# Performance work log

Measured on AMD Instinct MI355X. Metric: run time of the kernel, lower is better.

Reference implementation:

```python
import jax, jax.numpy as jnp
import numpy as np


def setup_inputs() -> dict:
    key = jax.random.key(0)
    k1, k2 = jax.random.split(key)
    B, C, H, W = 4, 64, 256, 512
    right_input = jax.random.normal(k1, (B, C, H, W), dtype=jnp.float32)
    disparity_samples = jax.random.uniform(k2, (B, 1, H, W), dtype=jnp.float32)
    return {"right_input": right_input, "disparity_samples": disparity_samples}


def reference(right_input, disparity_samples):
    B, C, H, W = right_input.shape
    dt = right_input.dtype
    # left pixel x-coordinates along width, broadcast over B,1,H
    left_y = jnp.arange(W, dtype=dt).reshape(1, 1, 1, W)
    right_y = left_y + disparity_samples                      # [B,1,H,W]
    ry_a = jnp.floor(right_y)
    ry_b = ry_a + 1.0
    wa = ry_b - right_y                                       # [B,1,H,W]
    wb = right_y - ry_a
    idx_a = jnp.clip(ry_a, 0, W - 1).astype(jnp.int32)
    idx_b = jnp.clip(ry_b, 0, W - 1).astype(jnp.int32)
    # broadcast indices across channels and gather along width (dim=3)
    idx_a = jnp.broadcast_to(idx_a, (B, C, H, W))
    idx_b = jnp.broadcast_to(idx_b, (B, C, H, W))
    feat_a = jnp.take_along_axis(right_input, idx_a, axis=3)
    feat_b = jnp.take_along_axis(right_input, idx_b, axis=3)
    warped = wa * feat_a + wb * feat_b                        # weights broadcast over C
    # zero out samples whose (unclamped) coordinate fell outside [0, W-1]
    oob = (right_y < 0).astype(dt) + (right_y > (W - 1)).astype(dt)
    return (1.0 - oob) * warped
```

## Files before the change

kernel.cpp:

```cpp
#include <hip/hip_runtime.h>

constexpr int B = 4;
constexpr int C = 64;
constexpr int H = 256;
constexpr int W = 512;

__global__ __launch_bounds__(256) void spatial_warp_kernel(
    const float* __restrict__ input,
    const float* __restrict__ disp,
    float* __restrict__ out)
{
    const long long tid  = (long long)blockIdx.x * blockDim.x + threadIdx.x;
    const long long idx4 = tid * 4;
    if (idx4 >= (long long)B * C * H * W) return;

    const int w0 = (int)(idx4 % W);
    long long rest = idx4 / W;
    const int h = (int)(rest % H);
    rest /= H;
    const int c = (int)(rest % C);
    const int b = (int)(rest / C);

    const long long pix = ((long long)b * H + h) * W + w0;
    const float4 d4 = *reinterpret_cast<const float4*>(disp + pix);

    const float* __restrict__ row =
        input + (((long long)b * C + c) * H + h) * (long long)W;

    const float dv[4] = {d4.x, d4.y, d4.z, d4.w};
    float ov[4];

#pragma unroll
    for (int i = 0; i < 4; ++i) {
        const float ry  = (float)(w0 + i) + dv[i];
        const float ra  = floorf(ry);
        const float rb  = ra + 1.0f;
        const float wa_ = rb - ry;
        const float wb_ = ry - ra;
        const float ra_c = fminf(fmaxf(ra, 0.0f), (float)(W - 1));
        const float rb_c = fminf(fmaxf(rb, 0.0f), (float)(W - 1));
        const int ia = (int)ra_c;
        const int ib = (int)rb_c;
        const float fa = row[ia];
        const float fb = row[ib];
        const float val = wa_ * fa + wb_ * fb;
        const bool valid = (ry >= 0.0f) && (ry <= (float)(W - 1));
        ov[i] = valid ? val : 0.0f;
    }

    float4 o;
    o.x = ov[0]; o.y = ov[1]; o.z = ov[2]; o.w = ov[3];
    *reinterpret_cast<float4*>(out + idx4) = o;
}

extern "C" void kernel_launch(void* const* d_in, const int* in_sizes, int n_in,
                              void* d_out, int out_size, void* d_ws, size_t ws_size,
                              hipStream_t stream) {
    const float* input = (const float*)d_in[0];
    const float* disp  = (const float*)d_in[1];
    float* out = (float*)d_out;

    const long long total   = (long long)B * C * H * W;
    const long long threads = total / 4;
    const int block = 256;
    const int grid  = (int)((threads + block - 1) / block);

    spatial_warp_kernel<<<grid, block, 0, stream>>>(input, disp, out);
}
```

Baseline: 253.6 us.

## Stage input rows in LDS and reuse disparity weights across channel groups

Each block now handles one (b,h) row for 16 channels. It loads the disparity row once into shared memory and computes the interpolation indices, weights and masks once per thread, then reuses them for every channel. Each channel row is brought in with coalesced float4 loads into LDS, and the two gathers read from LDS instead of global memory. This removes repeated disparity reads, the 64-bit index division and scattered global gathers. In exchange it adds two barriers per iteration and leaves little memory-level parallelism per thread.

```diff
diff --git a/kernel.cpp b/kernel.cpp
--- a/kernel.cpp
+++ b/kernel.cpp
@@ -4,53 +4,69 @@
 constexpr int C = 64;
 constexpr int H = 256;
 constexpr int W = 512;
+constexpr int CH_PER_BLOCK = 16;
+constexpr int ROWS_PER_ITER = 2;
 
 __global__ __launch_bounds__(256) void spatial_warp_kernel(
     const float* __restrict__ input,
     const float* __restrict__ disp,
     float* __restrict__ out)
 {
-    const long long tid  = (long long)blockIdx.x * blockDim.x + threadIdx.x;
-    const long long idx4 = tid * 4;
-    if (idx4 >= (long long)B * C * H * W) return;
+    __shared__ float s_row[ROWS_PER_ITER * W];
+    __shared__ float s_disp[W];
 
-    const int w0 = (int)(idx4 % W);
-    long long rest = idx4 / W;
-    const int h = (int)(rest % H);
-    rest /= H;
-    const int c = (int)(rest % C);
-    const int b = (int)(rest / C);
+    const int t = threadIdx.x;
+    const int cg = blockIdx.x % (C / CH_PER_BLOCK);
+    int rest = blockIdx.x / (C / CH_PER_BLOCK);
+    const int h = rest % H;
+    const int b = rest / H;
+    const int c_base = cg * CH_PER_BLOCK;
 
-    const long long pix = ((long long)b * H + h) * W + w0;
-    const float4 d4 = *reinterpret_cast<const float4*>(disp + pix);
+    const long long pix_base = ((long long)b * H + h) * W;
+    if (t < W / 4) {
+        reinterpret_cast<float4*>(s_disp)[t] =
+            reinterpret_cast<const float4*>(disp + pix_base)[t];
+    }
+    __syncthreads();
 
-    const float* __restrict__ row =
-        input + (((long long)b * C + c) * H + h) * (long long)W;
+    const int r     = t >> 7;
+    const int lane7 = t & 127;
 
-    const float dv[4] = {d4.x, d4.y, d4.z, d4.w};
-    float ov[4];
-
+    float wa4[4], wb4[4], msk[4];
+    int   ia4[4], ib4[4];
 #pragma unroll
     for (int i = 0; i < 4; ++i) {
-        const float ry  = (float)(w0 + i) + dv[i];
-        const float ra  = floorf(ry);
-        const float rb  = ra + 1.0f;
-        const float wa_ = rb - ry;
-        const float wb_ = ry - ra;
-        const float ra_c = fminf(fmaxf(ra, 0.0f), (float)(W - 1));
-        const float rb_c = fminf(fmaxf(rb, 0.0f), (float)(W - 1));
-        const int ia = (int)ra_c;
-        const int ib = (int)rb_c;
-        const float fa = row[ia];
-        const float fb = row[ib];
-        const float val = wa_ * fa + wb_ * fb;
-        const bool valid = (ry >= 0.0f) && (ry <= (float)(W - 1));
-        ov[i] = valid ? val : 0.0f;
+        const int w  = lane7 + 128 * i;
+        const float d  = s_disp[w];
+        const float ry = (float)w + d;
+        const float ra = floorf(ry);
+        const float rb = ra + 1.0f;
+        wa4[i] = rb - ry;
+        wb4[i] = ry - ra;
+        ia4[i] = (int)fminf(fmaxf(ra, 0.0f), (float)(W - 1));
+        ib4[i] = (int)fminf(fmaxf(rb, 0.0f), (float)(W - 1));
+        msk[i] = (ry >= 0.0f && ry <= (float)(W - 1)) ? 1.0f : 0.0f;
     }
 
-    float4 o;
-    o.x = ov[0]; o.y = ov[1]; o.z = ov[2]; o.w = ov[3];
-    *reinterpret_cast<float4*>(out + idx4) = o;
+    const int lds_base = r * W;
+#pragma unroll 2
+    for (int cc = 0; cc < CH_PER_BLOCK / ROWS_PER_ITER; ++cc) {
+        const int c_mine = c_base + cc * ROWS_PER_ITER + r;
+        const float* rowg = input + (((long long)b * C + c_mine) * H + h) * (long long)W;
+        const float4 v = reinterpret_cast<const float4*>(rowg)[lane7];
+        __syncthreads();
+        reinterpret_cast<float4*>(s_row + lds_base)[lane7] = v;
+        __syncthreads();
+
+        float* outg = out + (((long long)b * C + c_mine) * H + h) * (long long)W;
+#pragma unroll
+        for (int i = 0; i < 4; ++i) {
+            const int w = lane7 + 128 * i;
+            const float fa = s_row[lds_base + ia4[i]];
+            const float fb = s_row[lds_base + ib4[i]];
+            outg[w] = msk[i] * (wa4[i] * fa + wb4[i] * fb);
+        }
+    }
 }
 
 extern "C" void kernel_launch(void* const* d_in, const int* in_sizes, int n_in,
@@ -58,12 +74,8 @@
                               hipStream_t stream) {
     const float* input = (const float*)d_in[0];
     const float* disp  = (const float*)d_in[1];
-    float* out = (float*)d_out;
+    float* outp = (float*)d_out;
 
-    const long long total   = (long long)B * C * H * W;
-    const long long threads = total / 4;
-    const int block = 256;
-    const int grid  = (int)((threads + block - 1) / block);
-
-    spatial_warp_kernel<<<grid, block, 0, stream>>>(input, disp, out);
+    const int grid = B * H * (C / CH_PER_BLOCK);
+    spatial_warp_kernel<<<grid, 256, 0, stream>>>(input, disp, outp);
 }
```

After: 234.5 us. 7.5% less time.
